# Optimization experiments

Hardware: AMD Instinct MI355X
Metric: run time of the kernel (lower is better)

The kernel has to match this reference:

```python
import jax, jax.numpy as jnp
import numpy as np

N_NODES = 100000
N_EDGES = 1000000
VOCAB = 128
EMB = 64
HID = 64
N_CLASSES = 2
N_GRAPHS = 2048


def setup_inputs() -> dict:
    key = jax.random.key(0)
    ks = jax.random.split(key, 12)
    x = jax.random.randint(ks[0], (N_NODES,), 0, VOCAB)
    edge_index = jax.random.randint(ks[1], (2, N_EDGES), 0, N_NODES)
    batch = jnp.sort(jax.random.randint(ks[2], (N_NODES,), 0, N_GRAPHS))

    def glorot(k, shape):
        fan = shape[0]
        return jax.random.normal(k, shape, dtype=jnp.float32) / np.sqrt(fan).astype(np.float32)

    emb = jax.random.normal(ks[3], (VOCAB, EMB), dtype=jnp.float32)
    W1_l = glorot(ks[4], (EMB, HID)); b1 = jnp.zeros((HID,), jnp.float32)
    W1_r = glorot(ks[5], (EMB, HID))
    W2_l = glorot(ks[6], (HID, HID)); b2 = jnp.zeros((HID,), jnp.float32)
    W2_r = glorot(ks[7], (HID, HID))
    W_out = glorot(ks[8], (HID, N_CLASSES)); b_out = jnp.zeros((N_CLASSES,), jnp.float32)
    return {"x": x, "edge_index": edge_index, "batch": batch, "emb": emb,
            "W1_l": W1_l, "b1": b1, "W1_r": W1_r,
            "W2_l": W2_l, "b2": b2, "W2_r": W2_r,
            "W_out": W_out, "b_out": b_out}


def _sage_conv(h, src, dst, Wl, bl, Wr):
    # PyG SAGEConv: out = lin_l(mean_{j in N(i)} h_j) + lin_r(h_i); lin_r has no bias
    msgs = h[src]                                                        # [E, D] gather
    agg = jax.ops.segment_sum(msgs, dst, num_segments=N_NODES)          # [N, D] scatter-add
    cnt = jax.ops.segment_sum(jnp.ones((src.shape[0], 1), h.dtype), dst,
                              num_segments=N_NODES)                      # [N, 1] degree
    mean = agg / jnp.maximum(cnt, 1.0)
    return mean @ Wl + bl + h @ Wr


def reference(x, edge_index, batch, emb, W1_l, b1, W1_r, W2_l, b2, W2_r, W_out, b_out):
    src, dst = edge_index[0], edge_index[1]
    h = emb[x]                                                           # [N, EMB]
    h = jax.nn.relu(_sage_conv(h, src, dst, W1_l, b1, W1_r))             # [N, HID]
    h = jax.nn.relu(_sage_conv(h, src, dst, W2_l, b2, W2_r))             # [N, HID]
    # global_mean_pool over graph ids
    gsum = jax.ops.segment_sum(h, batch, num_segments=N_GRAPHS)          # [G, HID]
    gcnt = jax.ops.segment_sum(jnp.ones((N_NODES, 1), h.dtype), batch,
                               num_segments=N_GRAPHS)
    pooled = gsum / jnp.maximum(gcnt, 1.0)
    return pooled @ W_out + b_out                                        # [G, C]
```

## Files before the change

kernel.cpp:

```cpp
#include <hip/hip_runtime.h>
#include <hip/hip_bf16.h>

#define N_NODES 100000
#define N_EDGES 1000000
#define EMB 64
#define HID 64
#define VOCAB 128
#define N_GRAPHS 2048

#define CBUCKET 256
#define NBK ((N_NODES + CBUCKET - 1) / CBUCKET)
#define CAP 4096
#define CHUNK 4096
#define SCAT_BLOCKS ((N_EDGES + CHUNK - 1) / CHUNK)
#define GB ((N_NODES + 255) / 256)

#define BCASTF(v, l) __int_as_float(__builtin_amdgcn_readlane(__float_as_int(v), (l)))

typedef __attribute__((ext_vector_type(8))) short short8;
typedef __attribute__((ext_vector_type(4))) float f32x4;

__device__ __forceinline__ float bf2f(unsigned short u) {
    return __uint_as_float((unsigned)u << 16);
}
__device__ __forceinline__ unsigned short f2bf(float f) {
    return __bfloat16_as_ushort(__float2bfloat16(f));
}

__global__ __launch_bounds__(256) void scatter_kernel(
    const int* __restrict__ src, const int* __restrict__ dst,
    const int* __restrict__ x,
    int* __restrict__ cursor, unsigned* __restrict__ edge8,
    const int* __restrict__ batch, int* __restrict__ gstart,
    const float* __restrict__ emb, const float* __restrict__ W1l,
    const float* __restrict__ W1r,
    const float* __restrict__ W2l, const float* __restrict__ W2r,
    float* __restrict__ embW1l, float* __restrict__ embW1r,
    unsigned short* __restrict__ w2frag)
{
    __shared__ unsigned earr[CHUNK];
    __shared__ unsigned short karr[CHUNK];
    __shared__ int bcnt[NBK];
    __shared__ int bbase[NBK];
    int b = blockIdx.x;
    int t = threadIdx.x;

    if (b < SCAT_BLOCKS) {
        for (int i = t; i < NBK; i += 256) bcnt[i] = 0;
        __syncthreads();
        int e0 = b * CHUNK;
        int n = min(e0 + CHUNK, N_EDGES) - e0;
        for (int i = t; i < n; i += 256) {
            int d = dst[e0 + i];
            int s = src[e0 + i];
            int xv = x[s];
            int k = d >> 8;
            earr[i] = (unsigned)s | ((unsigned)xv << 17) | ((unsigned)(d & 255) << 24);
            karr[i] = (unsigned short)k;
            atomicAdd(&bcnt[k], 1);
        }
        __syncthreads();
        for (int i = t; i < NBK; i += 256) {
            int c = bcnt[i];
            bbase[i] = i * CAP + (c ? atomicAdd(&cursor[i], c) : 0);
            bcnt[i] = 0;
        }
        __syncthreads();
        for (int i = t; i < n; i += 256) {
            int k = karr[i];
            int off = atomicAdd(&bcnt[k], 1);
            edge8[bbase[k] + off] = earr[i];
        }
    } else if (b < SCAT_BLOCKS + GB) {
        int i = (b - SCAT_BLOCKS) * 256 + t;
        if (i >= N_NODES) return;
        int bg = batch[i];
        int bp = (i == 0) ? -1 : batch[i - 1];
        for (int g = bp + 1; g <= bg; ++g) gstart[g] = i;
        if (i == N_NODES - 1)
            for (int g = bg + 1; g <= N_GRAPHS; ++g) gstart[g] = N_NODES;
    } else {
        int vb = b - SCAT_BLOCKS - GB;
        int wave = t >> 6, lane = t & 63;
        int v = vb * 4 + wave;
        if (v < VOCAB) {
            float er = emb[v * 64 + lane];
            float al = 0.f, ar = 0.f;
#pragma unroll 8
            for (int d = 0; d < 64; ++d) {
                float e = BCASTF(er, d);
                al += e * W1l[d * 64 + lane];
                ar += e * W1r[d * 64 + lane];
            }
            embW1l[v * 64 + lane] = al;
            embW1r[v * 64 + lane] = ar;
        }
        int g = vb * 256 + t;
        int j = g & 7, l = (g >> 3) & 63, h = (g >> 9) & 1, tt = g >> 10;
        int k = h * 32 + ((l >> 4) * 8) + j;
        int n = tt * 16 + (l & 15);
        float w = (n < 64) ? W2l[k * 64 + n] : W2r[k * 64 + (n - 64)];
        w2frag[g] = f2bf(w);
    }
}

__global__ __launch_bounds__(256) void csr_kernel(
    const unsigned* __restrict__ edge8, const int* __restrict__ cursor,
    int* __restrict__ row_start, int* __restrict__ deg, int* __restrict__ col)
{
    __shared__ int cnt[CBUCKET];
    __shared__ int scn[CBUCKET];
    int b = blockIdx.x;
    int t = threadIdx.x;
    int lo = b * CAP, hi = lo + cursor[b];
    cnt[t] = 0;
    __syncthreads();
    for (int i = lo + t; i < hi; i += 256)
        atomicAdd(&cnt[edge8[i] >> 24], 1);
    __syncthreads();
    int v = cnt[t];
    scn[t] = v;
    __syncthreads();
    for (int off = 1; off < 256; off <<= 1) {
        int tmp = (t >= off) ? scn[t - off] : 0;
        __syncthreads();
        scn[t] += tmp;
        __syncthreads();
    }
    int excl = scn[t] - v;
    int node = b * CBUCKET + t;
    if (node < N_NODES) { row_start[node] = lo + excl; deg[node] = v; }
    cnt[t] = excl;
    __syncthreads();
    for (int i = lo + t; i < hi; i += 256) {
        unsigned e = edge8[i];
        int slot = atomicAdd(&cnt[e >> 24], 1);
        col[lo + slot] = (int)(e & 0xFFFFFF);
    }
}

#define S1_NPW 8
__global__ __launch_bounds__(256) void sage1_kernel(
    const int* __restrict__ x, const float* __restrict__ embW1l,
    const float* __restrict__ embW1r, const float* __restrict__ b1,
    const int* __restrict__ row_start, const int* __restrict__ deg,
    const int* __restrict__ col, const unsigned short* __restrict__ w2frag,
    unsigned char* __restrict__ p8, unsigned short* __restrict__ q16)
{
    __shared__ float elds[VOCAB * 64];
    int t = threadIdx.x;
    for (int i = t * 4; i < VOCAB * 64; i += 1024)
        *(float4*)&elds[i] = *(const float4*)&embW1l[i];
    __syncthreads();

    int wave = t >> 6, lane = t & 63;
    int block_base = blockIdx.x * (4 * S1_NPW);
    int base_node = block_base + wave * S1_NPW;
    int c = lane & 15;
    int g = lane >> 4;
    float4 bias4 = ((const float4*)b1)[c];

    int rs[S1_NPW], dgs[S1_NPW], cidx[S1_NPW], xn[S1_NPW];
    float4 self4[S1_NPW];
#pragma unroll
    for (int n = 0; n < S1_NPW; ++n) {
        rs[n] = row_start[base_node + n];
        dgs[n] = deg[base_node + n];
        xn[n] = x[base_node + n];
    }
#pragma unroll
    for (int n = 0; n < S1_NPW; ++n) {
        cidx[n] = (lane < dgs[n]) ? col[rs[n] + lane] : 0;
        self4[n] = ((const float4*)(embW1r + xn[n] * 64))[c];
    }

    unsigned short* msbuf = (unsigned short*)elds;
    ushort4 h1row[S1_NPW];

    for (int n = 0; n < S1_NPW; ++n) {
        int dg = dgs[n];
        int dgc = (dg < 64) ? dg : 64;

        float4 a0 = {0.f,0.f,0.f,0.f}, a1 = {0.f,0.f,0.f,0.f};
        for (int j = 0; j < dgc; j += 8) {
            int jj0 = j + g, jj1 = j + 4 + g;
            int x0 = __shfl(cidx[n], jj0, 64) >> 17;
            int x1 = __shfl(cidx[n], jj1, 64) >> 17;
            float4 v0 = *(const float4*)&elds[x0 * 64 + c * 4];
            float4 v1 = *(const float4*)&elds[x1 * 64 + c * 4];
            if (jj0 < dgc) { a0.x += v0.x; a0.y += v0.y; a0.z += v0.z; a0.w += v0.w; }
            if (jj1 < dgc) { a1.x += v1.x; a1.y += v1.y; a1.z += v1.z; a1.w += v1.w; }
        }
        for (int k = 64; k < dg; ++k) {
            int cc = col[rs[n] + k] >> 17;
            float4 v = *(const float4*)&elds[cc * 64 + c * 4];
            if (g == 0) { a0.x += v.x; a0.y += v.y; a0.z += v.z; a0.w += v.w; }
        }
        float sx = a0.x + a1.x, sy = a0.y + a1.y, sz = a0.z + a1.z, sw = a0.w + a1.w;
        sx += __shfl_xor(sx, 16, 64); sx += __shfl_xor(sx, 32, 64);
        sy += __shfl_xor(sy, 16, 64); sy += __shfl_xor(sy, 32, 64);
        sz += __shfl_xor(sz, 16, 64); sz += __shfl_xor(sz, 32, 64);
        sw += __shfl_xor(sw, 16, 64); sw += __shfl_xor(sw, 32, 64);

        float inv = 1.0f / fmaxf((float)dg, 1.0f);
        h1row[n].x = f2bf(fmaxf(sx * inv + bias4.x + self4[n].x, 0.f));
        h1row[n].y = f2bf(fmaxf(sy * inv + bias4.y + self4[n].y, 0.f));
        h1row[n].z = f2bf(fmaxf(sz * inv + bias4.z + self4[n].z, 0.f));
        h1row[n].w = f2bf(fmaxf(sw * inv + bias4.w + self4[n].w, 0.f));
    }
    __syncthreads();

    if (g == 0) {
#pragma unroll
        for (int n = 0; n < S1_NPW; ++n)
            *(ushort4*)&msbuf[(wave * S1_NPW + n) * 72 + c * 4] = h1row[n];
    }
    __syncthreads();

    int grp = wave >> 1, tbase = (wave & 1) * 4;
    int m = lane & 15, quad = lane >> 4;
    int base16g = block_base + grp * 16;
    const unsigned short* arow = &msbuf[(grp * 16 + m) * 72 + quad * 8];
    short8 a0 = *(const short8*)(arow);
    short8 a1 = *(const short8*)(arow + 32);

#pragma unroll
    for (int tt = tbase; tt < tbase + 4; ++tt) {
        short8 b0 = *(const short8*)(w2frag + tt * 1024 + lane * 8);
        short8 b1v = *(const short8*)(w2frag + tt * 1024 + 512 + lane * 8);
        f32x4 acc = {0.f, 0.f, 0.f, 0.f};
        acc = __builtin_amdgcn_mfma_f32_16x16x32_bf16(a0, b0, acc, 0, 0, 0);
        acc = __builtin_amdgcn_mfma_f32_16x16x32_bf16(a1, b1v, acc, 0, 0, 0);
        int o = tt * 16 + m;
        if (o < 64) {
            int pk01 = __builtin_amdgcn_cvt_pk_fp8_f32(acc[0], acc[1], 0, false);
            int pk23 = __builtin_amdgcn_cvt_pk_fp8_f32(acc[2], acc[3], 0, false);
            p8[(base16g + quad * 4 + 0) * 64 + o] = (unsigned char)(pk01 & 0xff);
            p8[(base16g + quad * 4 + 1) * 64 + o] = (unsigned char)((pk01 >> 8) & 0xff);
            p8[(base16g + quad * 4 + 2) * 64 + o] = (unsigned char)(pk23 & 0xff);
            p8[(base16g + quad * 4 + 3) * 64 + o] = (unsigned char)((pk23 >> 8) & 0xff);
        } else {
            int oc = o & 63;
#pragma unroll
            for (int i = 0; i < 4; ++i)
                q16[(base16g + quad * 4 + i) * 64 + oc] = f2bf(acc[i]);
        }
    }
}

#define S2_NPW 8
__global__ __launch_bounds__(256, 6) void sage2_kernel(
    const unsigned char* __restrict__ p, const unsigned short* __restrict__ q,
    const int* __restrict__ row_start, const int* __restrict__ deg,
    const int* __restrict__ col, const float* __restrict__ b2,
    const float* __restrict__ Wout, const int* __restrict__ batch,
    float* __restrict__ gsum)
{
    int t = threadIdx.x;
    int wave = t >> 6, lane = t & 63;
    int base_node = (blockIdx.x * 4 + wave) * S2_NPW;
    int c = lane & 15;
    int g = lane >> 4;

    float4 b2v = ((const float4*)b2)[c];
    float4 w01 = ((const float4*)Wout)[c * 2];
    float4 w23 = ((const float4*)Wout)[c * 2 + 1];

    int rs[S2_NPW], dgs[S2_NPW], cidx[S2_NPW];
#pragma unroll
    for (int n = 0; n < S2_NPW; ++n) {
        rs[n] = row_start[base_node + n];
        dgs[n] = deg[base_node + n];
    }
#pragma unroll
    for (int n = 0; n < S2_NPW; ++n)
        cidx[n] = (lane < dgs[n]) ? (col[rs[n] + lane] & 0x1FFFF) : 0;

    for (int n = 0; n < S2_NPW; ++n) {
        int node = base_node + n;
        int dg = dgs[n];
        int dgc = (dg < 64) ? dg : 64;

        float4 a0 = {0.f,0.f,0.f,0.f}, a1 = {0.f,0.f,0.f,0.f};
        for (int j = 0; j < dgc; j += 8) {
            int jj0 = j + g, jj1 = j + 4 + g;
            int i0 = __shfl(cidx[n], jj0, 64);
            int i1 = __shfl(cidx[n], jj1, 64);
            unsigned v0 = *(const unsigned*)(p + i0 * 64 + c * 4);
            unsigned v1 = *(const unsigned*)(p + i1 * 64 + c * 4);
            if (jj0 < dgc) {
                a0.x += __builtin_amdgcn_cvt_f32_fp8(v0, 0);
                a0.y += __builtin_amdgcn_cvt_f32_fp8(v0, 1);
                a0.z += __builtin_amdgcn_cvt_f32_fp8(v0, 2);
                a0.w += __builtin_amdgcn_cvt_f32_fp8(v0, 3);
            }
            if (jj1 < dgc) {
                a1.x += __builtin_amdgcn_cvt_f32_fp8(v1, 0);
                a1.y += __builtin_amdgcn_cvt_f32_fp8(v1, 1);
                a1.z += __builtin_amdgcn_cvt_f32_fp8(v1, 2);
                a1.w += __builtin_amdgcn_cvt_f32_fp8(v1, 3);
            }
        }
        for (int k = 64; k < dg; ++k) {
            int r = col[rs[n] + k] & 0x1FFFF;
            unsigned v = *(const unsigned*)(p + r * 64 + c * 4);
            if (g == 0) {
                a0.x += __builtin_amdgcn_cvt_f32_fp8(v, 0);
                a0.y += __builtin_amdgcn_cvt_f32_fp8(v, 1);
                a0.z += __builtin_amdgcn_cvt_f32_fp8(v, 2);
                a0.w += __builtin_amdgcn_cvt_f32_fp8(v, 3);
            }
        }
        float sx = a0.x + a1.x, sy = a0.y + a1.y, sz = a0.z + a1.z, sw = a0.w + a1.w;
        sx += __shfl_xor(sx, 16, 64); sx += __shfl_xor(sx, 32, 64);
        sy += __shfl_xor(sy, 16, 64); sy += __shfl_xor(sy, 32, 64);
        sz += __shfl_xor(sz, 16, 64); sz += __shfl_xor(sz, 32, 64);
        sw += __shfl_xor(sw, 16, 64); sw += __shfl_xor(sw, 32, 64);

        float inv = 1.0f / fmaxf((float)dg, 1.0f);
        ushort4 qv = *(const ushort4*)(q + node * 64 + c * 4);
        float h0 = fmaxf(sx * inv + b2v.x + bf2f(qv.x), 0.f);
        float h1 = fmaxf(sy * inv + b2v.y + bf2f(qv.y), 0.f);
        float h2 = fmaxf(sz * inv + b2v.z + bf2f(qv.z), 0.f);
        float h3 = fmaxf(sw * inv + b2v.w + bf2f(qv.w), 0.f);

        float p0 = h0 * w01.x + h1 * w01.z + h2 * w23.x + h3 * w23.z;
        float p1 = h0 * w01.y + h1 * w01.w + h2 * w23.y + h3 * w23.w;
        if (g != 0) { p0 = 0.f; p1 = 0.f; }
        p0 += __shfl_down(p0, 8, 64);  p1 += __shfl_down(p1, 8, 64);
        p0 += __shfl_down(p0, 4, 64);  p1 += __shfl_down(p1, 4, 64);
        p0 += __shfl_down(p0, 2, 64);  p1 += __shfl_down(p1, 2, 64);
        p0 += __shfl_down(p0, 1, 64);  p1 += __shfl_down(p1, 1, 64);
        if (lane == 0) {
            int grp = batch[node];
            atomicAdd(&gsum[grp * 2 + 0], p0);
            atomicAdd(&gsum[grp * 2 + 1], p1);
        }
    }
}

__global__ __launch_bounds__(256) void finalize_kernel(
    const float* __restrict__ gsum, const int* __restrict__ gstart,
    const float* __restrict__ bout, float* __restrict__ out)
{
    int g = blockIdx.x * 256 + threadIdx.x;
    if (g >= N_GRAPHS) return;
    int cnt = gstart[g + 1] - gstart[g];
    float inv = 1.0f / fmaxf((float)cnt, 1.0f);
    out[g * 2 + 0] = gsum[g * 2 + 0] * inv + bout[0];
    out[g * 2 + 1] = gsum[g * 2 + 1] * inv + bout[1];
}

extern "C" void kernel_launch(void* const* d_in, const int* in_sizes, int n_in,
                              void* d_out, int out_size, void* d_ws, size_t ws_size,
                              hipStream_t stream) {
    const int*   x    = (const int*)  d_in[0];
    const int*   ei   = (const int*)  d_in[1];
    const int*   batch= (const int*)  d_in[2];
    const float* emb  = (const float*)d_in[3];
    const float* W1l  = (const float*)d_in[4];
    const float* b1   = (const float*)d_in[5];
    const float* W1r  = (const float*)d_in[6];
    const float* W2l  = (const float*)d_in[7];
    const float* b2   = (const float*)d_in[8];
    const float* W2r  = (const float*)d_in[9];
    const float* Wout = (const float*)d_in[10];
    const float* bout = (const float*)d_in[11];
    float* out = (float*)d_out;

    const int* src = ei;
    const int* dst = ei + N_EDGES;

    char* ws = (char*)d_ws;
    size_t off = 0;
    unsigned char*  p8     = (unsigned char*) (ws + off); off += (size_t)N_NODES * 64;
    unsigned short* q16    = (unsigned short*)(ws + off); off += (size_t)N_NODES * 64 * 2;
    unsigned short* w2frag = (unsigned short*)(ws + off); off += (size_t)8192 * 2;
    float*    embW1l = (float*)   (ws + off); off += (size_t)VOCAB * 64 * 4;
    float*    embW1r = (float*)   (ws + off); off += (size_t)VOCAB * 64 * 4;
    int*      rowst  = (int*)     (ws + off); off += (size_t)N_NODES * 4;
    int*      deg    = (int*)     (ws + off); off += (size_t)N_NODES * 4;
    int*      col    = (int*)     (ws + off); off += (size_t)(NBK * CAP + 256) * 4;
    unsigned* edge8  = (unsigned*)(ws + off); off += (size_t)NBK * CAP * 4;
    int*      gstart = (int*)     (ws + off); off += (size_t)(N_GRAPHS + 1) * 4;
    int*      cursor = (int*)     (ws + off); off += (size_t)NBK * 4;
    float*    gsum   = (float*)   (ws + off); off += (size_t)N_GRAPHS * 2 * 4;

    hipMemsetAsync(cursor, 0, (size_t)NBK * 4 + (size_t)N_GRAPHS * 2 * 4, stream);

    scatter_kernel<<<SCAT_BLOCKS + GB + 32, 256, 0, stream>>>(
        src, dst, x, cursor, edge8,
        batch, gstart, emb, W1l, W1r, W2l, W2r, embW1l, embW1r, w2frag);
    csr_kernel<<<NBK, 256, 0, stream>>>(edge8, cursor, rowst, deg, col);
    sage1_kernel<<<N_NODES / (4 * S1_NPW), 256, 0, stream>>>(
        x, embW1l, embW1r, b1, rowst, deg, col, w2frag, p8, q16);
    sage2_kernel<<<N_NODES / (4 * S2_NPW), 256, 0, stream>>>(
        p8, q16, rowst, deg, col, b2, Wout, batch, gsum);
    finalize_kernel<<<(N_GRAPHS + 255) / 256, 256, 0, stream>>>(gsum, gstart, bout, out);
}
```

Baseline: 209.5 us.

## Remap sage2 to eight lanes per node with wide fp8 gathers

```diff
diff --git a/kernel.cpp b/kernel.cpp
--- a/kernel.cpp
+++ b/kernel.cpp
@@ -19,6 +19,8 @@
 
 typedef __attribute__((ext_vector_type(8))) short short8;
 typedef __attribute__((ext_vector_type(4))) float f32x4;
+typedef __attribute__((ext_vector_type(2))) float f32x2;
+typedef __attribute__((ext_vector_type(2))) unsigned int uint2v;
 
 __device__ __forceinline__ float bf2f(unsigned short u) {
     return __uint_as_float((unsigned)u << 16);
@@ -26,6 +28,8 @@
 __device__ __forceinline__ unsigned short f2bf(float f) {
     return __bfloat16_as_ushort(__float2bfloat16(f));
 }
+
+#define SWZF(x, patt) __int_as_float(__builtin_amdgcn_ds_swizzle(__float_as_int(x), (patt)))
 
 __global__ __launch_bounds__(256) void scatter_kernel(
     const int* __restrict__ src, const int* __restrict__ dst,
@@ -36,7 +40,7 @@
     const float* __restrict__ W1r,
     const float* __restrict__ W2l, const float* __restrict__ W2r,
     float* __restrict__ embW1l, float* __restrict__ embW1r,
-    unsigned short* __restrict__ w2frag)
+    unsigned short* __restrict__ w2frag, unsigned char* __restrict__ p8z)
 {
     __shared__ unsigned earr[CHUNK];
     __shared__ unsigned short karr[CHUNK];
@@ -81,6 +85,8 @@
             for (int g = bg + 1; g <= N_GRAPHS; ++g) gstart[g] = N_NODES;
     } else {
         int vb = b - SCAT_BLOCKS - GB;
+        if (vb == 0 && t < 16)
+            ((unsigned*)(p8z + (size_t)N_NODES * 64))[t] = 0u;
         int wave = t >> 6, lane = t & 63;
         int v = vb * 4 + wave;
         if (v < VOCAB) {
@@ -248,7 +254,6 @@
     }
 }
 
-#define S2_NPW 8
 __global__ __launch_bounds__(256, 6) void sage2_kernel(
     const unsigned char* __restrict__ p, const unsigned short* __restrict__ q,
     const int* __restrict__ row_start, const int* __restrict__ deg,
@@ -258,84 +263,66 @@
 {
     int t = threadIdx.x;
     int wave = t >> 6, lane = t & 63;
-    int base_node = (blockIdx.x * 4 + wave) * S2_NPW;
-    int c = lane & 15;
-    int g = lane >> 4;
-
-    float4 b2v = ((const float4*)b2)[c];
-    float4 w01 = ((const float4*)Wout)[c * 2];
-    float4 w23 = ((const float4*)Wout)[c * 2 + 1];
-
-    int rs[S2_NPW], dgs[S2_NPW], cidx[S2_NPW];
-#pragma unroll
-    for (int n = 0; n < S2_NPW; ++n) {
-        rs[n] = row_start[base_node + n];
-        dgs[n] = deg[base_node + n];
-    }
-#pragma unroll
-    for (int n = 0; n < S2_NPW; ++n)
-        cidx[n] = (lane < dgs[n]) ? (col[rs[n] + lane] & 0x1FFFF) : 0;
-
-    for (int n = 0; n < S2_NPW; ++n) {
-        int node = base_node + n;
-        int dg = dgs[n];
-        int dgc = (dg < 64) ? dg : 64;
-
-        float4 a0 = {0.f,0.f,0.f,0.f}, a1 = {0.f,0.f,0.f,0.f};
-        for (int j = 0; j < dgc; j += 8) {
-            int jj0 = j + g, jj1 = j + 4 + g;
-            int i0 = __shfl(cidx[n], jj0, 64);
-            int i1 = __shfl(cidx[n], jj1, 64);
-            unsigned v0 = *(const unsigned*)(p + i0 * 64 + c * 4);
-            unsigned v1 = *(const unsigned*)(p + i1 * 64 + c * 4);
-            if (jj0 < dgc) {
-                a0.x += __builtin_amdgcn_cvt_f32_fp8(v0, 0);
-                a0.y += __builtin_amdgcn_cvt_f32_fp8(v0, 1);
-                a0.z += __builtin_amdgcn_cvt_f32_fp8(v0, 2);
-                a0.w += __builtin_amdgcn_cvt_f32_fp8(v0, 3);
-            }
-            if (jj1 < dgc) {
-                a1.x += __builtin_amdgcn_cvt_f32_fp8(v1, 0);
-                a1.y += __builtin_amdgcn_cvt_f32_fp8(v1, 1);
-                a1.z += __builtin_amdgcn_cvt_f32_fp8(v1, 2);
-                a1.w += __builtin_amdgcn_cvt_f32_fp8(v1, 3);
-            }
-        }
-        for (int k = 64; k < dg; ++k) {
-            int r = col[rs[n] + k] & 0x1FFFF;
-            unsigned v = *(const unsigned*)(p + r * 64 + c * 4);
-            if (g == 0) {
-                a0.x += __builtin_amdgcn_cvt_f32_fp8(v, 0);
-                a0.y += __builtin_amdgcn_cvt_f32_fp8(v, 1);
-                a0.z += __builtin_amdgcn_cvt_f32_fp8(v, 2);
-                a0.w += __builtin_amdgcn_cvt_f32_fp8(v, 3);
-            }
-        }
-        float sx = a0.x + a1.x, sy = a0.y + a1.y, sz = a0.z + a1.z, sw = a0.w + a1.w;
-        sx += __shfl_xor(sx, 16, 64); sx += __shfl_xor(sx, 32, 64);
-        sy += __shfl_xor(sy, 16, 64); sy += __shfl_xor(sy, 32, 64);
-        sz += __shfl_xor(sz, 16, 64); sz += __shfl_xor(sz, 32, 64);
-        sw += __shfl_xor(sw, 16, 64); sw += __shfl_xor(sw, 32, 64);
-
-        float inv = 1.0f / fmaxf((float)dg, 1.0f);
-        ushort4 qv = *(const ushort4*)(q + node * 64 + c * 4);
-        float h0 = fmaxf(sx * inv + b2v.x + bf2f(qv.x), 0.f);
-        float h1 = fmaxf(sy * inv + b2v.y + bf2f(qv.y), 0.f);
-        float h2 = fmaxf(sz * inv + b2v.z + bf2f(qv.z), 0.f);
-        float h3 = fmaxf(sw * inv + b2v.w + bf2f(qv.w), 0.f);
-
-        float p0 = h0 * w01.x + h1 * w01.z + h2 * w23.x + h3 * w23.z;
-        float p1 = h0 * w01.y + h1 * w01.w + h2 * w23.y + h3 * w23.w;
-        if (g != 0) { p0 = 0.f; p1 = 0.f; }
-        p0 += __shfl_down(p0, 8, 64);  p1 += __shfl_down(p1, 8, 64);
-        p0 += __shfl_down(p0, 4, 64);  p1 += __shfl_down(p1, 4, 64);
-        p0 += __shfl_down(p0, 2, 64);  p1 += __shfl_down(p1, 2, 64);
-        p0 += __shfl_down(p0, 1, 64);  p1 += __shfl_down(p1, 1, 64);
-        if (lane == 0) {
-            int grp = batch[node];
-            atomicAdd(&gsum[grp * 2 + 0], p0);
-            atomicAdd(&gsum[grp * 2 + 1], p1);
-        }
+    int c8 = lane & 7;
+    int node = (blockIdx.x * 4 + wave) * 8 + (lane >> 3);
+
+    int rs = row_start[node];
+    int dg = deg[node];
+    int grp = batch[node];
+
+    float4 accA = {0.f,0.f,0.f,0.f}, accB = {0.f,0.f,0.f,0.f};
+    int r0 = 0;
+    while (true) {
+        int cid0 = (r0 + c8     < dg) ? (col[rs + r0 + c8    ] & 0x1FFFF) : N_NODES;
+        int cid1 = (r0 + c8 + 8 < dg) ? (col[rs + r0 + c8 + 8] & 0x1FFFF) : N_NODES;
+
+        uint2v v[16];
+#define GATHER(r, cidv, slot) { \
+        int i_ = __builtin_amdgcn_ds_swizzle((cidv), (((r) << 5) | 0x18)); \
+        v[slot] = *(const uint2v*)(p + ((size_t)i_ << 6) + (c8 << 3)); }
+        GATHER(0, cid0, 0)  GATHER(1, cid0, 1)  GATHER(2, cid0, 2)  GATHER(3, cid0, 3)
+        GATHER(4, cid0, 4)  GATHER(5, cid0, 5)  GATHER(6, cid0, 6)  GATHER(7, cid0, 7)
+        GATHER(0, cid1, 8)  GATHER(1, cid1, 9)  GATHER(2, cid1, 10) GATHER(3, cid1, 11)
+        GATHER(4, cid1, 12) GATHER(5, cid1, 13) GATHER(6, cid1, 14) GATHER(7, cid1, 15)
+#undef GATHER
+
+#pragma unroll
+        for (int r = 0; r < 16; ++r) {
+            f32x2 f01 = __builtin_amdgcn_cvt_pk_f32_fp8((int)v[r].x, false);
+            f32x2 f23 = __builtin_amdgcn_cvt_pk_f32_fp8((int)v[r].x, true);
+            f32x2 f45 = __builtin_amdgcn_cvt_pk_f32_fp8((int)v[r].y, false);
+            f32x2 f67 = __builtin_amdgcn_cvt_pk_f32_fp8((int)v[r].y, true);
+            accA.x += f01.x; accA.y += f01.y; accA.z += f23.x; accA.w += f23.y;
+            accB.x += f45.x; accB.y += f45.y; accB.z += f67.x; accB.w += f67.y;
+        }
+        r0 += 16;
+        if (r0 >= dg) break;
+    }
+
+    float inv = 1.0f / fmaxf((float)dg, 1.0f);
+    const float4* b2p = (const float4*)b2 + (c8 << 1);
+    float4 b2a = b2p[0], b2b = b2p[1];
+    short8 qv = *(const short8*)(q + ((size_t)node << 6) + (c8 << 3));
+    float h0 = fmaxf(accA.x * inv + b2a.x + bf2f((unsigned short)qv[0]), 0.f);
+    float h1 = fmaxf(accA.y * inv + b2a.y + bf2f((unsigned short)qv[1]), 0.f);
+    float h2 = fmaxf(accA.z * inv + b2a.z + bf2f((unsigned short)qv[2]), 0.f);
+    float h3 = fmaxf(accA.w * inv + b2a.w + bf2f((unsigned short)qv[3]), 0.f);
+    float h4 = fmaxf(accB.x * inv + b2b.x + bf2f((unsigned short)qv[4]), 0.f);
+    float h5 = fmaxf(accB.y * inv + b2b.y + bf2f((unsigned short)qv[5]), 0.f);
+    float h6 = fmaxf(accB.z * inv + b2b.z + bf2f((unsigned short)qv[6]), 0.f);
+    float h7 = fmaxf(accB.w * inv + b2b.w + bf2f((unsigned short)qv[7]), 0.f);
+
+    const float4* wv = (const float4*)Wout + (c8 << 2);
+    float4 wa = wv[0], wb = wv[1], wc = wv[2], wd = wv[3];
+    float s0 = h0*wa.x + h1*wa.z + h2*wb.x + h3*wb.z + h4*wc.x + h5*wc.z + h6*wd.x + h7*wd.z;
+    float s1 = h0*wa.y + h1*wa.w + h2*wb.y + h3*wb.w + h4*wc.y + h5*wc.w + h6*wd.y + h7*wd.w;
+
+    s0 += SWZF(s0, 0x101F); s1 += SWZF(s1, 0x101F);
+    s0 += SWZF(s0, 0x081F); s1 += SWZF(s1, 0x081F);
+    s0 += SWZF(s0, 0x041F); s1 += SWZF(s1, 0x041F);
+    if (c8 == 0) {
+        atomicAdd(&gsum[(grp << 1) + 0], s0);
+        atomicAdd(&gsum[(grp << 1) + 1], s1);
     }
 }
 
@@ -373,7 +360,7 @@
 
     char* ws = (char*)d_ws;
     size_t off = 0;
-    unsigned char*  p8     = (unsigned char*) (ws + off); off += (size_t)N_NODES * 64;
+    unsigned char*  p8     = (unsigned char*) (ws + off); off += (size_t)N_NODES * 64 + 64;
     unsigned short* q16    = (unsigned short*)(ws + off); off += (size_t)N_NODES * 64 * 2;
     unsigned short* w2frag = (unsigned short*)(ws + off); off += (size_t)8192 * 2;
     float*    embW1l = (float*)   (ws + off); off += (size_t)VOCAB * 64 * 4;
@@ -390,11 +377,11 @@
 
     scatter_kernel<<<SCAT_BLOCKS + GB + 32, 256, 0, stream>>>(
         src, dst, x, cursor, edge8,
-        batch, gstart, emb, W1l, W1r, W2l, W2r, embW1l, embW1r, w2frag);
+        batch, gstart, emb, W1l, W1r, W2l, W2r, embW1l, embW1r, w2frag, p8);
     csr_kernel<<<NBK, 256, 0, stream>>>(edge8, cursor, rowst, deg, col);
     sage1_kernel<<<N_NODES / (4 * S1_NPW), 256, 0, stream>>>(
         x, embW1l, embW1r, b1, rowst, deg, col, w2frag, p8, q16);
-    sage2_kernel<<<N_NODES / (4 * S2_NPW), 256, 0, stream>>>(
+    sage2_kernel<<<N_NODES / 32, 256, 0, stream>>>(
         p8, q16, rowst, deg, col, b2, Wout, batch, gsum);
     finalize_kernel<<<(N_GRAPHS + 255) / 256, 256, 0, stream>>>(gsum, gstart, bout, out);
 }
```

Measured after the change: 222.1 us. +6.0%, slower.

## Batch two nodes per iteration in sage2 with zero-row padding for branchless gathers

Applied to the files above, without the earlier changes.

```diff
diff --git a/kernel.cpp b/kernel.cpp
--- a/kernel.cpp
+++ b/kernel.cpp
@@ -19,6 +19,7 @@
 
 typedef __attribute__((ext_vector_type(8))) short short8;
 typedef __attribute__((ext_vector_type(4))) float f32x4;
+typedef __attribute__((ext_vector_type(2))) float f32x2;
 
 __device__ __forceinline__ float bf2f(unsigned short u) {
     return __uint_as_float((unsigned)u << 16);
@@ -36,7 +37,7 @@
     const float* __restrict__ W1r,
     const float* __restrict__ W2l, const float* __restrict__ W2r,
     float* __restrict__ embW1l, float* __restrict__ embW1r,
-    unsigned short* __restrict__ w2frag)
+    unsigned short* __restrict__ w2frag, unsigned char* __restrict__ p8z)
 {
     __shared__ unsigned earr[CHUNK];
     __shared__ unsigned short karr[CHUNK];
@@ -81,6 +82,8 @@
             for (int g = bg + 1; g <= N_GRAPHS; ++g) gstart[g] = N_NODES;
     } else {
         int vb = b - SCAT_BLOCKS - GB;
+        if (vb == 0 && t < 16)
+            ((unsigned*)(p8z + (size_t)N_NODES * 64))[t] = 0u;
         int wave = t >> 6, lane = t & 63;
         int v = vb * 4 + wave;
         if (v < VOCAB) {
@@ -249,6 +252,7 @@
 }
 
 #define S2_NPW 8
+#define ZROW N_NODES
 __global__ __launch_bounds__(256, 6) void sage2_kernel(
     const unsigned char* __restrict__ p, const unsigned short* __restrict__ q,
     const int* __restrict__ row_start, const int* __restrict__ deg,
@@ -274,69 +278,99 @@
     }
 #pragma unroll
     for (int n = 0; n < S2_NPW; ++n)
-        cidx[n] = (lane < dgs[n]) ? (col[rs[n] + lane] & 0x1FFFF) : 0;
-
-    for (int n = 0; n < S2_NPW; ++n) {
-        int node = base_node + n;
-        int dg = dgs[n];
-        int dgc = (dg < 64) ? dg : 64;
-
-        float4 a0 = {0.f,0.f,0.f,0.f}, a1 = {0.f,0.f,0.f,0.f};
-        for (int j = 0; j < dgc; j += 8) {
-            int jj0 = j + g, jj1 = j + 4 + g;
-            int i0 = __shfl(cidx[n], jj0, 64);
-            int i1 = __shfl(cidx[n], jj1, 64);
-            unsigned v0 = *(const unsigned*)(p + i0 * 64 + c * 4);
-            unsigned v1 = *(const unsigned*)(p + i1 * 64 + c * 4);
-            if (jj0 < dgc) {
-                a0.x += __builtin_amdgcn_cvt_f32_fp8(v0, 0);
-                a0.y += __builtin_amdgcn_cvt_f32_fp8(v0, 1);
-                a0.z += __builtin_amdgcn_cvt_f32_fp8(v0, 2);
-                a0.w += __builtin_amdgcn_cvt_f32_fp8(v0, 3);
+        cidx[n] = (lane < dgs[n]) ? (col[rs[n] + lane] & 0x1FFFF) : ZROW;
+
+#define ACC(a, v) { f32x2 f01_ = __builtin_amdgcn_cvt_pk_f32_fp8((int)(v), false); \
+                    f32x2 f23_ = __builtin_amdgcn_cvt_pk_f32_fp8((int)(v), true);  \
+                    (a).x += f01_.x; (a).y += f01_.y; (a).z += f23_.x; (a).w += f23_.y; }
+
+#pragma unroll
+    for (int n = 0; n < S2_NPW; n += 2) {
+        int dgA = dgs[n], dgB = dgs[n + 1];
+
+        int iA0 = __shfl(cidx[n], g, 64);
+        int iA1 = __shfl(cidx[n], 4 + g, 64);
+        int iA2 = __shfl(cidx[n], 8 + g, 64);
+        int iA3 = __shfl(cidx[n], 12 + g, 64);
+        int iB0 = __shfl(cidx[n + 1], g, 64);
+        int iB1 = __shfl(cidx[n + 1], 4 + g, 64);
+        int iB2 = __shfl(cidx[n + 1], 8 + g, 64);
+        int iB3 = __shfl(cidx[n + 1], 12 + g, 64);
+
+        unsigned vA0 = *(const unsigned*)(p + (size_t)iA0 * 64 + c * 4);
+        unsigned vA1 = *(const unsigned*)(p + (size_t)iA1 * 64 + c * 4);
+        unsigned vA2 = *(const unsigned*)(p + (size_t)iA2 * 64 + c * 4);
+        unsigned vA3 = *(const unsigned*)(p + (size_t)iA3 * 64 + c * 4);
+        unsigned vB0 = *(const unsigned*)(p + (size_t)iB0 * 64 + c * 4);
+        unsigned vB1 = *(const unsigned*)(p + (size_t)iB1 * 64 + c * 4);
+        unsigned vB2 = *(const unsigned*)(p + (size_t)iB2 * 64 + c * 4);
+        unsigned vB3 = *(const unsigned*)(p + (size_t)iB3 * 64 + c * 4);
+
+        float4 aA = {0.f,0.f,0.f,0.f}, aB = {0.f,0.f,0.f,0.f};
+        ACC(aA, vA0) ACC(aA, vA1) ACC(aA, vA2) ACC(aA, vA3)
+        ACC(aB, vB0) ACC(aB, vB1) ACC(aB, vB2) ACC(aB, vB3)
+
+        for (int j = 16; j < dgA; j += 8) {
+            int i0 = __shfl(cidx[n], j + g, 64);
+            int i1 = __shfl(cidx[n], j + 4 + g, 64);
+            unsigned v0 = *(const unsigned*)(p + (size_t)i0 * 64 + c * 4);
+            unsigned v1 = *(const unsigned*)(p + (size_t)i1 * 64 + c * 4);
+            ACC(aA, v0) ACC(aA, v1)
+        }
+        for (int j = 16; j < dgB; j += 8) {
+            int i0 = __shfl(cidx[n + 1], j + g, 64);
+            int i1 = __shfl(cidx[n + 1], j + 4 + g, 64);
+            unsigned v0 = *(const unsigned*)(p + (size_t)i0 * 64 + c * 4);
+            unsigned v1 = *(const unsigned*)(p + (size_t)i1 * 64 + c * 4);
+            ACC(aB, v0) ACC(aB, v1)
+        }
+        for (int k = 64; k < dgA; ++k) {
+            int r = col[rs[n] + k] & 0x1FFFF;
+            unsigned v = *(const unsigned*)(p + (size_t)r * 64 + c * 4);
+            if (g == 0) ACC(aA, v)
+        }
+        for (int k = 64; k < dgB; ++k) {
+            int r = col[rs[n + 1] + k] & 0x1FFFF;
+            unsigned v = *(const unsigned*)(p + (size_t)r * 64 + c * 4);
+            if (g == 0) ACC(aB, v)
+        }
+
+        aA.x += __shfl_xor(aA.x, 16, 64); aA.y += __shfl_xor(aA.y, 16, 64);
+        aA.z += __shfl_xor(aA.z, 16, 64); aA.w += __shfl_xor(aA.w, 16, 64);
+        aB.x += __shfl_xor(aB.x, 16, 64); aB.y += __shfl_xor(aB.y, 16, 64);
+        aB.z += __shfl_xor(aB.z, 16, 64); aB.w += __shfl_xor(aB.w, 16, 64);
+        aA.x += __shfl_xor(aA.x, 32, 64); aA.y += __shfl_xor(aA.y, 32, 64);
+        aA.z += __shfl_xor(aA.z, 32, 64); aA.w += __shfl_xor(aA.w, 32, 64);
+        aB.x += __shfl_xor(aB.x, 32, 64); aB.y += __shfl_xor(aB.y, 32, 64);
+        aB.z += __shfl_xor(aB.z, 32, 64); aB.w += __shfl_xor(aB.w, 32, 64);
+
+#pragma unroll
+        for (int e = 0; e < 2; ++e) {
+            int node = base_node + n + e;
+            int dg = (e == 0) ? dgA : dgB;
+            float4 a = (e == 0) ? aA : aB;
+            float inv = 1.0f / fmaxf((float)dg, 1.0f);
+            ushort4 qv = *(const ushort4*)(q + node * 64 + c * 4);
+            float h0 = fmaxf(a.x * inv + b2v.x + bf2f(qv.x), 0.f);
+            float h1 = fmaxf(a.y * inv + b2v.y + bf2f(qv.y), 0.f);
+            float h2 = fmaxf(a.z * inv + b2v.z + bf2f(qv.z), 0.f);
+            float h3 = fmaxf(a.w * inv + b2v.w + bf2f(qv.w), 0.f);
+
+            float p0 = h0 * w01.x + h1 * w01.z + h2 * w23.x + h3 * w23.z;
+            float p1 = h0 * w01.y + h1 * w01.w + h2 * w23.y + h3 * w23.w;
+            if (g != 0) { p0 = 0.f; p1 = 0.f; }
+            p0 += __shfl_down(p0, 8, 64);  p1 += __shfl_down(p1, 8, 64);
+            p0 += __shfl_down(p0, 4, 64);  p1 += __shfl_down(p1, 4, 64);
+            p0 += __shfl_down(p0, 2, 64);  p1 += __shfl_down(p1, 2, 64);
+            p0 += __shfl_down(p0, 1, 64);  p1 += __shfl_down(p1, 1, 64);
+            if (lane == 0) {
+                int grp = batch[node];
+                atomicAdd(&gsum[grp * 2 + 0], p0);
+                atomicAdd(&gsum[grp * 2 + 1], p1);
             }
-            if (jj1 < dgc) {
-                a1.x += __builtin_amdgcn_cvt_f32_fp8(v1, 0);
-                a1.y += __builtin_amdgcn_cvt_f32_fp8(v1, 1);
-                a1.z += __builtin_amdgcn_cvt_f32_fp8(v1, 2);
-                a1.w += __builtin_amdgcn_cvt_f32_fp8(v1, 3);
-            }
-        }
-        for (int k = 64; k < dg; ++k) {
-            int r = col[rs[n] + k] & 0x1FFFF;
-            unsigned v = *(const unsigned*)(p + r * 64 + c * 4);
-            if (g == 0) {
-                a0.x += __builtin_amdgcn_cvt_f32_fp8(v, 0);
-                a0.y += __builtin_amdgcn_cvt_f32_fp8(v, 1);
-                a0.z += __builtin_amdgcn_cvt_f32_fp8(v, 2);
-                a0.w += __builtin_amdgcn_cvt_f32_fp8(v, 3);
-            }
-        }
-        float sx = a0.x + a1.x, sy = a0.y + a1.y, sz = a0.z + a1.z, sw = a0.w + a1.w;
-        sx += __shfl_xor(sx, 16, 64); sx += __shfl_xor(sx, 32, 64);
-        sy += __shfl_xor(sy, 16, 64); sy += __shfl_xor(sy, 32, 64);
-        sz += __shfl_xor(sz, 16, 64); sz += __shfl_xor(sz, 32, 64);
-        sw += __shfl_xor(sw, 16, 64); sw += __shfl_xor(sw, 32, 64);
-
-        float inv = 1.0f / fmaxf((float)dg, 1.0f);
-        ushort4 qv = *(const ushort4*)(q + node * 64 + c * 4);
-        float h0 = fmaxf(sx * inv + b2v.x + bf2f(qv.x), 0.f);
-        float h1 = fmaxf(sy * inv + b2v.y + bf2f(qv.y), 0.f);
-        float h2 = fmaxf(sz * inv + b2v.z + bf2f(qv.z), 0.f);
-        float h3 = fmaxf(sw * inv + b2v.w + bf2f(qv.w), 0.f);
-
-        float p0 = h0 * w01.x + h1 * w01.z + h2 * w23.x + h3 * w23.z;
-        float p1 = h0 * w01.y + h1 * w01.w + h2 * w23.y + h3 * w23.w;
-        if (g != 0) { p0 = 0.f; p1 = 0.f; }
-        p0 += __shfl_down(p0, 8, 64);  p1 += __shfl_down(p1, 8, 64);
-        p0 += __shfl_down(p0, 4, 64);  p1 += __shfl_down(p1, 4, 64);
-        p0 += __shfl_down(p0, 2, 64);  p1 += __shfl_down(p1, 2, 64);
-        p0 += __shfl_down(p0, 1, 64);  p1 += __shfl_down(p1, 1, 64);
-        if (lane == 0) {
-            int grp = batch[node];
-            atomicAdd(&gsum[grp * 2 + 0], p0);
-            atomicAdd(&gsum[grp * 2 + 1], p1);
-        }
-    }
+        }
+    }
+#undef ACC
 }
 
 __global__ __launch_bounds__(256) void finalize_kernel(
@@ -373,7 +407,7 @@
 
     char* ws = (char*)d_ws;
     size_t off = 0;
-    unsigned char*  p8     = (unsigned char*) (ws + off); off += (size_t)N_NODES * 64;
+    unsigned char*  p8     = (unsigned char*) (ws + off); off += (size_t)N_NODES * 64 + 64;
     unsigned short* q16    = (unsigned short*)(ws + off); off += (size_t)N_NODES * 64 * 2;
     unsigned short* w2frag = (unsigned short*)(ws + off); off += (size_t)8192 * 2;
     float*    embW1l = (float*)   (ws + off); off += (size_t)VOCAB * 64 * 4;
@@ -390,7 +424,7 @@
 
     scatter_kernel<<<SCAT_BLOCKS + GB + 32, 256, 0, stream>>>(
         src, dst, x, cursor, edge8,
-        batch, gstart, emb, W1l, W1r, W2l, W2r, embW1l, embW1r, w2frag);
+        batch, gstart, emb, W1l, W1r, W2l, W2r, embW1l, embW1r, w2frag, p8);
     csr_kernel<<<NBK, 256, 0, stream>>>(edge8, cursor, rowst, deg, col);
     sage1_kernel<<<N_NODES / (4 * S1_NPW), 256, 0, stream>>>(
         x, embW1l, embW1r, b1, rowst, deg, col, w2frag, p8, q16);
```

Result: no change. 209.2 us (-0.1%).
